# Performance work log

Measured on AMD Instinct MI355X. Metric: run time of the kernel, lower is better.

Reference implementation:

```python
import jax, jax.numpy as jnp
import numpy as np

# ---- static grid config (matches init_kwargs: xmin=[0,0], xmax=[2,2], margin=0.1, ppu=64) ----
XMIN = np.array([0.0, 0.0], dtype=np.float32)
XMAX = np.array([2.0, 2.0], dtype=np.float32)
MARGIN = 0.1
PPU = 64
INIT_LENGTHSCALE = 0.1


def _make_grid():
    # half number of points per dim, rounded up to a power of 2
    half_n = np.ceil((0.5 * (XMAX - XMIN) + MARGIN) * PPU)
    half_n = (2.0 ** np.ceil(np.log2(half_n))).astype(np.int64)  # [128, 128]
    x_mid = 0.5 * (XMIN + XMAX)
    axes = [x_mid[d] + np.arange(-half_n[d], half_n[d], dtype=np.float32) / PPU
            for d in range(len(XMIN))]
    mesh = np.meshgrid(*axes, indexing="ij")
    return jnp.asarray(np.stack(mesh, axis=-1))  # [256, 256, 2]


def setup_inputs() -> dict:
    key = jax.random.key(0)
    k1, k2, k3 = jax.random.split(key, 3)
    m, nc, nt, dx, dy = 2, 1024, 128, 2, 16
    xc = jax.random.uniform(k1, (m, nc, dx), dtype=jnp.float32) * 2.0  # in [0, 2)
    yc = jax.random.normal(k2, (m, nc, dy), dtype=jnp.float32)
    xt = jax.random.uniform(k3, (m, nt, dx), dtype=jnp.float32) * 2.0
    # lengthscale_param = log(exp(init_lengthscale) - 1) per dim (softplus inverse)
    lengthscale_param = jnp.log(jnp.expm1(jnp.full((dx,), INIT_LENGTHSCALE, dtype=jnp.float32)))
    return {"xc": xc, "yc": yc, "xt": xt, "lengthscale_param": lengthscale_param}


def _compute_eq_weights(x1, x2, lengthscales):
    # x1: [m, n1, dx], x2: [m, n2, dx] -> exp(-0.5 * sum_d ((x1-x2)/l)^2): [m, n1, n2]
    a = x1 / lengthscales
    b = x2 / lengthscales
    sq = (jnp.sum(a * a, -1)[:, :, None]
          + jnp.sum(b * b, -1)[:, None, :]
          - 2.0 * jnp.einsum("mid,mjd->mij", a, b))
    return jnp.exp(-0.5 * sq)


def reference(xc, yc, xt, lengthscale_param):
    m = xc.shape[0]
    # append ones channel (density channel)
    yc = jnp.concatenate([yc, jnp.ones(yc.shape[:-1] + (1,), yc.dtype)], axis=-1)
    lengthscale = 1e-05 + jax.nn.softplus(lengthscale_param)  # [dx]
    x_grid = _make_grid()  # [256, 256, 2]
    x_grid_b = jnp.broadcast_to(x_grid, (m,) + x_grid.shape)  # [m, 256, 256, 2]
    x_grid_flat = x_grid_b.reshape(m, -1, x_grid.shape[-1])  # [m, ng, dx]
    weights = _compute_eq_weights(x_grid_flat, xc, lengthscale)  # [m, ng, nc]
    z_grid_flat = weights @ yc  # [m, ng, dy+1]
    z_grid = z_grid_flat.reshape(x_grid_b.shape[:-1] + (z_grid_flat.shape[-1],))
    return (x_grid_b, z_grid)
```

## Files before the change

### kernel.cpp

```cpp
#include <hip/hip_runtime.h>

#define NC 1024
#define DY 16
#define NG 65536

#define SZ_WXH (256 * 1024)
#define SZ_WYA (16 * 32 * 64 * 8)
#define SZ_YTB (32 * 64 * 8)

typedef float v4f __attribute__((ext_vector_type(4)));
typedef _Float16 h8 __attribute__((ext_vector_type(8)));

__global__ __launch_bounds__(256) void setconv_tables(
    const float* __restrict__ xc, const float* __restrict__ yc,
    const float* __restrict__ lsp,
    _Float16* __restrict__ WXh, _Float16* __restrict__ WYA,
    _Float16* __restrict__ YTB, int m)
{
    const int t  = blockIdx.x * 256 + threadIdx.x;
    const int T0 = m * (SZ_WXH / 8);
    const int T1 = T0 + m * (SZ_WYA / 8);
    const int T2 = T1 + m * (SZ_YTB / 8);
    if (t >= T2) return;

    if (t < T0) {
        const float l0 = 1e-5f + __logf(1.0f + __expf(lsp[0]));
        const float s0 = 0.84932184f / l0;
        const int mm  = t >> 15;
        const int rem = t & 32767;
        const int i   = rem >> 7;
        const int k0  = (rem & 127) << 3;
        const float g = (1.0f + (float)(i - 128) * 0.015625f) * s0;
        h8 o;
#pragma unroll
        for (int jj = 0; jj < 8; ++jj) {
            const float u = g - xc[((size_t)(mm * NC + k0 + jj)) << 1] * s0;
            o[jj] = (_Float16)__builtin_amdgcn_exp2f(-u * u);
        }
        *(h8*)&WXh[(size_t)t * 8] = o;
    } else if (t < T1) {
        const float l1 = 1e-5f + __logf(1.0f + __expf(lsp[1]));
        const float s1 = 0.84932184f / l1;
        const int tt   = t - T0;
        const int mm   = tt >> 15;
        const int rem  = tt & 32767;
        const int jt   = rem >> 11;
        const int ks   = (rem >> 6) & 31;
        const int lane = rem & 63;
        const int j    = jt * 16 + (lane & 15);
        const int k0   = ks * 32 + ((lane >> 4) << 3);
        const float g  = (1.0f + (float)(j - 128) * 0.015625f) * s1;
        h8 o;
#pragma unroll
        for (int jj = 0; jj < 8; ++jj) {
            const float u = g - xc[(((size_t)(mm * NC + k0 + jj)) << 1) + 1] * s1;
            o[jj] = (_Float16)__builtin_amdgcn_exp2f(-u * u);
        }
        *(h8*)&WYA[(size_t)tt * 8] = o;
    } else {
        const int tt   = t - T1;
        const int mm   = tt >> 11;
        const int rem  = tt & 2047;
        const int ks   = rem >> 6;
        const int lane = rem & 63;
        const int ch   = lane & 15;
        const int k0   = ks * 32 + ((lane >> 4) << 3);
        h8 o;
#pragma unroll
        for (int jj = 0; jj < 8; ++jj)
            o[jj] = (_Float16)yc[(((size_t)(mm * NC + k0 + jj)) << 4) + ch];
        *(h8*)&YTB[(size_t)tt * 8] = o;
    }
}

__global__ __launch_bounds__(256, 2) void setconv_main(
    const _Float16* __restrict__ WXh, const _Float16* __restrict__ WYA,
    const _Float16* __restrict__ YTB,
    float* __restrict__ out_grid,
    float* __restrict__ out_z)
{
    __shared__ __align__(16) _Float16 ytb[SZ_YTB];
    __shared__ __align__(16) _Float16 wx4[4][NC];

    const int mi   = blockIdx.y;
    const int bx   = blockIdx.x;
    const int ig   = bx >> 2;
    const int jg   = bx & 3;
    const int tid  = threadIdx.x;
    const int wave = tid >> 6;
    const int lane = tid & 63;
    const int q    = lane >> 4;
    const int r    = lane & 15;
    const int jt   = jg * 4 + wave;
    const int i0   = ig * 4;

    {
        const int g  = (i0 + (tid >> 6)) * 256 + jg * 64 + (tid & 63);
        const float gx = 1.0f + (float)((g >> 8) - 128) * 0.015625f;
        const float gy = 1.0f + (float)((g & 255) - 128) * 0.015625f;
        ((float2*)out_grid)[(size_t)mi * NG + g] = make_float2(gx, gy);
    }

    {
        const float4* wsrc = (const float4*)(WXh + ((size_t)mi * 256 + i0) * 1024);
        float4* wdst = (float4*)wx4;
        wdst[tid]       = wsrc[tid];
        wdst[tid + 256] = wsrc[tid + 256];
        const float4* src = (const float4*)(YTB + (size_t)mi * SZ_YTB);
        float4* dst = (float4*)ytb;
#pragma unroll
        for (int tt = 0; tt < 8; ++tt) dst[tid + 256 * tt] = src[tid + 256 * tt];
    }
    __syncthreads();

    const _Float16* wyp = WYA + (((size_t)mi * 16 + jt) * 32 * 64 + lane) * 8;

    h8 ones;
#pragma unroll
    for (int e = 0; e < 8; ++e) ones[e] = (_Float16)1.0f;

    v4f accD[4], accS[4];
#pragma unroll
    for (int ii = 0; ii < 4; ++ii) {
        accD[ii] = (v4f){0.f, 0.f, 0.f, 0.f};
        accS[ii] = (v4f){0.f, 0.f, 0.f, 0.f};
    }

#pragma unroll 4
    for (int ks = 0; ks < 32; ++ks) {
        const h8 wy = *(const h8*)(wyp + (size_t)ks * 512);
        const h8 yt = *(const h8*)&ytb[((size_t)ks * 64 + lane) * 8];
#pragma unroll
        for (int ii = 0; ii < 4; ++ii) {
            const h8 wx = *(const h8*)&wx4[ii][ks * 32 + q * 8];
            const h8 a  = wy * wx;
            accD[ii] = __builtin_amdgcn_mfma_f32_16x16x32_f16(a, yt,   accD[ii], 0, 0, 0);
            accS[ii] = __builtin_amdgcn_mfma_f32_16x16x32_f16(a, ones, accS[ii], 0, 0, 0);
        }
    }

#pragma unroll
    for (int ii = 0; ii < 4; ++ii) {
        float* __restrict__ oz =
            out_z + ((size_t)mi * NG + (size_t)(i0 + ii) * 256 + jt * 16) * 17;
#pragma unroll
        for (int reg = 0; reg < 4; ++reg) {
            const int row = q * 4 + reg;
            oz[(size_t)row * 17 + r] = accD[ii][reg];
            if (r == 0) oz[(size_t)row * 17 + 16] = accS[ii][reg];
        }
    }
}

extern "C" void kernel_launch(void* const* d_in, const int* in_sizes, int n_in,
                              void* d_out, int out_size, void* d_ws, size_t ws_size,
                              hipStream_t stream) {
    const float* xc  = (const float*)d_in[0];
    const float* yc  = (const float*)d_in[1];
    const float* lsp = (const float*)d_in[3];

    int m = in_sizes[0] / (NC * 2);

    float* out_grid = (float*)d_out;
    float* out_z    = (float*)d_out + (size_t)m * NG * 2;

    _Float16* WXh = (_Float16*)d_ws;
    _Float16* WYA = WXh + (size_t)m * SZ_WXH;
    _Float16* YTB = WYA + (size_t)m * SZ_WYA;

    const int total1 = m * (SZ_WXH / 8 + SZ_WYA / 8 + SZ_YTB / 8);
    hipLaunchKernelGGL(setconv_tables, dim3((total1 + 255) / 256), dim3(256),
                       0, stream, xc, yc, lsp, WXh, WYA, YTB, m);

    hipLaunchKernelGGL(setconv_main, dim3(256, m), dim3(256), 0, stream,
                       WXh, WYA, YTB, out_grid, out_z);
}
```

Before: 73.71 us.

## Compute separable Gaussian weight tables in-block and retile to 16x16 grid patches

The x- and y-direction exponential weight tables are no longer precomputed into global workspace by a separate kernel. Each block of the main kernel now computes its own 16-row x-table and 16-column y-table straight into shared memory, and only the fp16 yc table is still prepared by a small pre-kernel. Blocks cover 16x16 grid patches with one shared y-table for all waves, and yc is streamed from global memory. This removes the global writes and reads of roughly a megabyte of tables, at the cost of redundant exp evaluations across blocks and more setup work before the MFMA loop.

After: 76.37 us. +3.6%, slower.

```diff
diff --git a/kernel.cpp b/kernel.cpp
--- a/kernel.cpp
+++ b/kernel.cpp
@@ -4,116 +4,94 @@
 #define DY 16
 #define NG 65536
 
-#define SZ_WXH (256 * 1024)
-#define SZ_WYA (16 * 32 * 64 * 8)
 #define SZ_YTB (32 * 64 * 8)
 
 typedef float v4f __attribute__((ext_vector_type(4)));
 typedef _Float16 h8 __attribute__((ext_vector_type(8)));
 
-__global__ __launch_bounds__(256) void setconv_tables(
-    const float* __restrict__ xc, const float* __restrict__ yc,
-    const float* __restrict__ lsp,
-    _Float16* __restrict__ WXh, _Float16* __restrict__ WYA,
-    _Float16* __restrict__ YTB, int m)
+__global__ __launch_bounds__(256) void setconv_ytb(
+    const float* __restrict__ yc, _Float16* __restrict__ YTB, int m)
 {
-    const int t  = blockIdx.x * 256 + threadIdx.x;
-    const int T0 = m * (SZ_WXH / 8);
-    const int T1 = T0 + m * (SZ_WYA / 8);
-    const int T2 = T1 + m * (SZ_YTB / 8);
-    if (t >= T2) return;
-
-    if (t < T0) {
-        const float l0 = 1e-5f + __logf(1.0f + __expf(lsp[0]));
-        const float s0 = 0.84932184f / l0;
-        const int mm  = t >> 15;
-        const int rem = t & 32767;
-        const int i   = rem >> 7;
-        const int k0  = (rem & 127) << 3;
-        const float g = (1.0f + (float)(i - 128) * 0.015625f) * s0;
-        h8 o;
+    const int t = blockIdx.x * 256 + threadIdx.x;
+    if (t >= m * 2048) return;
+    const int mm   = t >> 11;
+    const int cell = t & 2047;
+    const int lane = cell & 63;
+    const int ks   = cell >> 6;
+    const int ch   = lane & 15;
+    const int k0   = ks * 32 + ((lane >> 4) << 3);
+    h8 o;
 #pragma unroll
-        for (int jj = 0; jj < 8; ++jj) {
-            const float u = g - xc[((size_t)(mm * NC + k0 + jj)) << 1] * s0;
-            o[jj] = (_Float16)__builtin_amdgcn_exp2f(-u * u);
-        }
-        *(h8*)&WXh[(size_t)t * 8] = o;
-    } else if (t < T1) {
-        const float l1 = 1e-5f + __logf(1.0f + __expf(lsp[1]));
-        const float s1 = 0.84932184f / l1;
-        const int tt   = t - T0;
-        const int mm   = tt >> 15;
-        const int rem  = tt & 32767;
-        const int jt   = rem >> 11;
-        const int ks   = (rem >> 6) & 31;
-        const int lane = rem & 63;
-        const int j    = jt * 16 + (lane & 15);
-        const int k0   = ks * 32 + ((lane >> 4) << 3);
-        const float g  = (1.0f + (float)(j - 128) * 0.015625f) * s1;
-        h8 o;
-#pragma unroll
-        for (int jj = 0; jj < 8; ++jj) {
-            const float u = g - xc[(((size_t)(mm * NC + k0 + jj)) << 1) + 1] * s1;
-            o[jj] = (_Float16)__builtin_amdgcn_exp2f(-u * u);
-        }
-        *(h8*)&WYA[(size_t)tt * 8] = o;
-    } else {
-        const int tt   = t - T1;
-        const int mm   = tt >> 11;
-        const int rem  = tt & 2047;
-        const int ks   = rem >> 6;
-        const int lane = rem & 63;
-        const int ch   = lane & 15;
-        const int k0   = ks * 32 + ((lane >> 4) << 3);
-        h8 o;
-#pragma unroll
-        for (int jj = 0; jj < 8; ++jj)
-            o[jj] = (_Float16)yc[(((size_t)(mm * NC + k0 + jj)) << 4) + ch];
-        *(h8*)&YTB[(size_t)tt * 8] = o;
-    }
+    for (int jj = 0; jj < 8; ++jj)
+        o[jj] = (_Float16)yc[(((size_t)(mm * NC + k0 + jj)) << 4) + ch];
+    *(h8*)&YTB[(size_t)t * 8] = o;
 }
 
 __global__ __launch_bounds__(256, 2) void setconv_main(
-    const _Float16* __restrict__ WXh, const _Float16* __restrict__ WYA,
+    const float* __restrict__ xc,
+    const float* __restrict__ lsp,
     const _Float16* __restrict__ YTB,
     float* __restrict__ out_grid,
     float* __restrict__ out_z)
 {
-    __shared__ __align__(16) _Float16 ytb[SZ_YTB];
-    __shared__ __align__(16) _Float16 wx4[4][NC];
+    __shared__ __align__(16) _Float16 wyA[2048 * 8];
+    __shared__ __align__(16) _Float16 wx16[16][NC];
 
     const int mi   = blockIdx.y;
     const int bx   = blockIdx.x;
-    const int ig   = bx >> 2;
-    const int jg   = bx & 3;
+    const int ig   = bx >> 4;
+    const int jg   = bx & 15;
     const int tid  = threadIdx.x;
     const int wave = tid >> 6;
     const int lane = tid & 63;
     const int q    = lane >> 4;
     const int r    = lane & 15;
-    const int jt   = jg * 4 + wave;
-    const int i0   = ig * 4;
+    const int i0   = ig * 16;
+    const int j0   = jg * 16;
+
+    const float l0 = 1e-5f + __logf(1.0f + __expf(lsp[0]));
+    const float l1 = 1e-5f + __logf(1.0f + __expf(lsp[1]));
+    const float R  = 0.84932184f;
+    const float s0 = R / l0, s1 = R / l1;
 
     {
-        const int g  = (i0 + (tid >> 6)) * 256 + jg * 64 + (tid & 63);
-        const float gx = 1.0f + (float)((g >> 8) - 128) * 0.015625f;
-        const float gy = 1.0f + (float)((g & 255) - 128) * 0.015625f;
-        ((float2*)out_grid)[(size_t)mi * NG + g] = make_float2(gx, gy);
+        const int i = i0 + (tid >> 4), j = j0 + (tid & 15);
+        const float gx = 1.0f + (float)(i - 128) * 0.015625f;
+        const float gy = 1.0f + (float)(j - 128) * 0.015625f;
+        ((float2*)out_grid)[(size_t)mi * NG + i * 256 + j] = make_float2(gx, gy);
     }
 
-    {
-        const float4* wsrc = (const float4*)(WXh + ((size_t)mi * 256 + i0) * 1024);
-        float4* wdst = (float4*)wx4;
-        wdst[tid]       = wsrc[tid];
-        wdst[tid + 256] = wsrc[tid + 256];
-        const float4* src = (const float4*)(YTB + (size_t)mi * SZ_YTB);
-        float4* dst = (float4*)ytb;
 #pragma unroll
-        for (int tt = 0; tt < 8; ++tt) dst[tid + 256 * tt] = src[tid + 256 * tt];
+    for (int c = 0; c < 8; ++c) {
+        const int cell = tid + 256 * c;
+        const int ks = cell >> 6, ln = cell & 63;
+        const int rr = ln & 15, qq = ln >> 4;
+        const int k0 = ks * 32 + qq * 8;
+        const float gy = (1.0f + (float)(j0 + rr - 128) * 0.015625f) * s1;
+        h8 o;
+#pragma unroll
+        for (int jj = 0; jj < 8; ++jj) {
+            const float u = gy - xc[(((size_t)mi * NC + k0 + jj) << 1) + 1] * s1;
+            o[jj] = (_Float16)__builtin_amdgcn_exp2f(-u * u);
+        }
+        *(h8*)&wyA[(size_t)cell * 8] = o;
+    }
+#pragma unroll
+    for (int c = 0; c < 8; ++c) {
+        const int idx = tid + 256 * c;
+        const int il = idx >> 7, k0 = (idx & 127) << 3;
+        const float gx = (1.0f + (float)(i0 + il - 128) * 0.015625f) * s0;
+        h8 o;
+#pragma unroll
+        for (int jj = 0; jj < 8; ++jj) {
+            const float u = gx - xc[((size_t)mi * NC + k0 + jj) << 1] * s0;
+            o[jj] = (_Float16)__builtin_amdgcn_exp2f(-u * u);
+        }
+        *(h8*)&wx16[0][idx * 8] = o;
     }
     __syncthreads();
 
-    const _Float16* wyp = WYA + (((size_t)mi * 16 + jt) * 32 * 64 + lane) * 8;
+    const _Float16* ytp = YTB + ((size_t)mi * 2048 + lane) * 8;
 
     h8 ones;
 #pragma unroll
@@ -128,11 +106,11 @@
 
 #pragma unroll 4
     for (int ks = 0; ks < 32; ++ks) {
-        const h8 wy = *(const h8*)(wyp + (size_t)ks * 512);
-        const h8 yt = *(const h8*)&ytb[((size_t)ks * 64 + lane) * 8];
+        const h8 yt = *(const h8*)(ytp + (size_t)ks * 512);
+        const h8 wy = *(const h8*)&wyA[((size_t)ks * 64 + lane) * 8];
 #pragma unroll
         for (int ii = 0; ii < 4; ++ii) {
-            const h8 wx = *(const h8*)&wx4[ii][ks * 32 + q * 8];
+            const h8 wx = *(const h8*)&wx16[wave * 4 + ii][ks * 32 + q * 8];
             const h8 a  = wy * wx;
             accD[ii] = __builtin_amdgcn_mfma_f32_16x16x32_f16(a, yt,   accD[ii], 0, 0, 0);
             accS[ii] = __builtin_amdgcn_mfma_f32_16x16x32_f16(a, ones, accS[ii], 0, 0, 0);
@@ -141,8 +119,8 @@
 
 #pragma unroll
     for (int ii = 0; ii < 4; ++ii) {
-        float* __restrict__ oz =
-            out_z + ((size_t)mi * NG + (size_t)(i0 + ii) * 256 + jt * 16) * 17;
+        const int i = i0 + wave * 4 + ii;
+        float* __restrict__ oz = out_z + ((size_t)mi * NG + (size_t)i * 256 + j0) * 17;
 #pragma unroll
         for (int reg = 0; reg < 4; ++reg) {
             const int row = q * 4 + reg;
@@ -164,14 +142,11 @@
     float* out_grid = (float*)d_out;
     float* out_z    = (float*)d_out + (size_t)m * NG * 2;
 
-    _Float16* WXh = (_Float16*)d_ws;
-    _Float16* WYA = WXh + (size_t)m * SZ_WXH;
-    _Float16* YTB = WYA + (size_t)m * SZ_WYA;
+    _Float16* YTB = (_Float16*)d_ws;
 
-    const int total1 = m * (SZ_WXH / 8 + SZ_WYA / 8 + SZ_YTB / 8);
-    hipLaunchKernelGGL(setconv_tables, dim3((total1 + 255) / 256), dim3(256),
-                       0, stream, xc, yc, lsp, WXh, WYA, YTB, m);
+    hipLaunchKernelGGL(setconv_ytb, dim3((m * 2048 + 255) / 256), dim3(256),
+                       0, stream, yc, YTB, m);
 
     hipLaunchKernelGGL(setconv_main, dim3(256, m), dim3(256), 0, stream,
-                       WXh, WYA, YTB, out_grid, out_z);
+                       xc, lsp, YTB, out_grid, out_z);
 }
```
